# Kernel tuning notes

Measured on AMD Instinct MI355X. Metric: run time of the kernel, lower is better.

## Reference

```python
import jax, jax.numpy as jnp
import numpy as np

NUM_CLASSES = 19  # configer.get('data','num_classes')


def _batch_label_vector(targets, num_classes, grid_size):
    # targets: [B, H, W] int labels in [0, num_classes)
    b, h, w = targets.shape
    pad_h = (-h) % grid_size
    pad_w = (-w) % grid_size
    # pad with value == num_classes, which torch.histc(min=0, max=num_classes-1)
    # ignores; we route it to an extra dustbin column and drop it.
    t = jnp.pad(targets, ((0, 0), (0, pad_h), (0, pad_w)),
                constant_values=num_classes)
    hh, ww = h + pad_h, w + pad_w
    # tile into (grid_size x grid_size) blocks -> [n_blocks, g*g]
    t = t.reshape(b, hh // grid_size, grid_size, ww // grid_size, grid_size)
    t = t.transpose(0, 1, 3, 2, 4).reshape(-1, grid_size * grid_size)
    n_blocks = t.shape[0]
    rows = jnp.arange(n_blocks)[:, None]  # [n_blocks, 1]
    # presence vector: hist > 0 <=> scatter-set ones at (block, label)
    tvect = jnp.zeros((n_blocks, num_classes + 1), jnp.float32)
    tvect = tvect.at[rows, t].set(1.0)
    return tvect[:, :num_classes]  # drop dustbin (pad value) column


def setup_inputs() -> dict:
    key = jax.random.key(0)
    k1, k2 = jax.random.split(key)
    B, H, W, G = 16, 1024, 2048, 8
    n_blocks = B * (H // G) * (W // G)  # 524288
    preds = jax.random.normal(k1, (n_blocks, NUM_CLASSES), jnp.float32)
    targets = jax.random.randint(k2, (B, H, W), 0, NUM_CLASSES, jnp.int32)
    return {"preds": preds, "targets": targets, "grid_size": G}


def reference(preds, targets, grid_size):
    se_target = _batch_label_vector(targets, NUM_CLASSES, grid_size)
    # BCELoss(sigmoid(preds), se_target), mean reduction.
    # Numerically stable: -log(sigmoid(x)) = softplus(-x),
    #                     -log(1-sigmoid(x)) = softplus(x)
    loss = se_target * jax.nn.softplus(-preds) + (1.0 - se_target) * jax.nn.softplus(preds)
    return jnp.mean(loss)
```

## Files before the change

### kernel.cpp

```cpp
#include <hip/hip_runtime.h>
#include <cmath>


#define NCLS 19

__global__ __launch_bounds__(256) void fsenc_loss_kernel(
    const float* __restrict__ preds,
    const int*   __restrict__ targets,
    float*       __restrict__ out,
    int B, int H, int W, float inv_count)
{
    const int t  = threadIdx.x;
    const int wg = blockIdx.x;

    const int strips_per_row = W / 1024;
    const int rows_per_img   = H / 8;
    const int block_row = wg / strips_per_row;
    const int strip     = wg % strips_per_row;
    const int b_img = block_row / rows_per_img;
    const int bh    = block_row % rows_per_img;
    const int col0  = strip * 1024;

    const int4* tgt4 = (const int4*)targets;
    const long row_stride4 = (long)W / 4;
    long base = ((long)(b_img * H + bh * 8) * W + col0) / 4 + t;

    unsigned mask = 0u;
    #pragma unroll
    for (int r = 0; r < 8; ++r) {
        int4 v = tgt4[base + (long)r * row_stride4];
        mask |= (1u << v.x) | (1u << v.y) | (1u << v.z) | (1u << v.w);
    }
    mask |= __shfl_xor(mask, 1);

    const int wpr = W / 8;
    const long blk = (long)(b_img * rows_per_img + bh) * wpr
                   + strip * 128 + (t >> 1);
    const float* row = preds + blk * NCLS;

    const int c0 = (t & 1) ? 10 : 0;
    const int c1 = (t & 1) ? NCLS : 10;
    float acc = 0.f;
    #pragma unroll
    for (int c = c0; c < c1; ++c) {
        float x  = row[c];
        float sp = fmaxf(x, 0.f) + log1pf(expf(-fabsf(x)));
        acc += sp - (((mask >> c) & 1u) ? x : 0.f);
    }

    #pragma unroll
    for (int off = 32; off; off >>= 1)
        acc += __shfl_down(acc, off);

    __shared__ float s[4];
    if ((t & 63) == 0) s[t >> 6] = acc;
    __syncthreads();
    if (t == 0) {
        float tot = s[0] + s[1] + s[2] + s[3];
        atomicAdd(out, tot * inv_count);
    }
}

extern "C" void kernel_launch(void* const* d_in, const int* in_sizes, int n_in,
                              void* d_out, int out_size, void* d_ws, size_t ws_size,
                              hipStream_t stream) {
    const float* preds   = (const float*)d_in[0];
    const int*   targets = (const int*)d_in[1];
    float*       out     = (float*)d_out;

    const int B = 16, H = 1024, W = 2048;
    const float inv_count = 1.0f / (float)in_sizes[0];

    hipMemsetAsync(out, 0, sizeof(float), stream);

    const int grid = B * (H / 8) * (W / 1024);
    fsenc_loss_kernel<<<grid, 256, 0, stream>>>(preds, targets, out,
                                                B, H, W, inv_count);
}
```

Baseline: 242.6 us.

## Stage label masks in LDS and read preds with coalesced float4 loads

Each workgroup now writes its 128 per-block label masks to shared memory and reads its contiguous 2432-float slice of preds as float4, so preds reads are coalesced instead of strided 19-float row reads per thread pair. Block and class indices are recovered with a multiply-shift division by 19. The softplus also moves to fast __expf/__logf intrinsics, which trades some accuracy for fewer instructions. The extra __syncthreads and LDS lookups add a little overhead, and the flat indexing assumes preds rows line up with the workgroup layout.

```diff
diff --git a/kernel.cpp b/kernel.cpp
--- a/kernel.cpp
+++ b/kernel.cpp
@@ -12,6 +12,9 @@
 {
     const int t  = threadIdx.x;
     const int wg = blockIdx.x;
+
+    __shared__ unsigned s_mask[128];
+    __shared__ float s_part[4];
 
     const int strips_per_row = W / 1024;
     const int rows_per_img   = H / 8;
@@ -32,31 +35,36 @@
         mask |= (1u << v.x) | (1u << v.y) | (1u << v.z) | (1u << v.w);
     }
     mask |= __shfl_xor(mask, 1);
+    if ((t & 1) == 0) s_mask[t >> 1] = mask;
+    __syncthreads();
 
-    const int wpr = W / 8;
-    const long blk = (long)(b_img * rows_per_img + bh) * wpr
-                   + strip * 128 + (t >> 1);
-    const float* row = preds + blk * NCLS;
+    const float4* p4 = (const float4*)(preds + (long)wg * 2432);
 
-    const int c0 = (t & 1) ? 10 : 0;
-    const int c1 = (t & 1) ? NCLS : 10;
     float acc = 0.f;
-    #pragma unroll
-    for (int c = c0; c < c1; ++c) {
-        float x  = row[c];
-        float sp = fmaxf(x, 0.f) + log1pf(expf(-fabsf(x)));
-        acc += sp - (((mask >> c) & 1u) ? x : 0.f);
+    for (int i = t; i < 608; i += 256) {
+        float4 v = p4[i];
+        const unsigned l0 = (unsigned)i * 4u;
+        float xs[4] = {v.x, v.y, v.z, v.w};
+        #pragma unroll
+        for (int k = 0; k < 4; ++k) {
+            unsigned l   = l0 + (unsigned)k;
+            unsigned blk = (l * 3450u) >> 16;
+            unsigned c   = l - blk * 19u;
+            float x  = xs[k];
+            float sp = fmaxf(x, 0.f) + __logf(1.f + __expf(-fabsf(x)));
+            float tf = (float)((s_mask[blk] >> c) & 1u);
+            acc += sp - tf * x;
+        }
     }
 
     #pragma unroll
     for (int off = 32; off; off >>= 1)
         acc += __shfl_down(acc, off);
 
-    __shared__ float s[4];
-    if ((t & 63) == 0) s[t >> 6] = acc;
+    if ((t & 63) == 0) s_part[t >> 6] = acc;
     __syncthreads();
     if (t == 0) {
-        float tot = s[0] + s[1] + s[2] + s[3];
+        float tot = s_part[0] + s_part[1] + s_part[2] + s_part[3];
         atomicAdd(out, tot * inv_count);
     }
 }
```

New measurement: 230.3 us. 5.1% less time.
